# Performance work log

Hardware: AMD Instinct MI355X
Metric: run time of the kernel (lower is better)

Reference implementation:

```python
import jax, jax.numpy as jnp
import numpy as np


def setup_inputs() -> dict:
    key = jax.random.key(0)
    ks = jax.random.split(key, 8)
    B, S, H = 16, 512, 1024
    K, E, L = 32, 1024, 2  # max_node_length, max_edge_length=K**2, num_labels
    seq = jax.random.normal(ks[0], (B, S, H), jnp.float32)
    # structured cumulative proof offsets: col0=1 ('<s>' offset, skipped by forward),
    # then n increasing offsets, zeros terminate. n <= K-1 so NAF node fits in K slots.
    rng = np.random.default_rng(0)
    off = np.zeros((B, K), np.int64)
    off[:, 0] = 1
    for b in range(B):
        n = int(rng.integers(8, K))  # 8..31 segment nodes
        lens = rng.integers(4, 14, size=n)
        off[b, 1:n + 1] = np.cumsum(lens)  # max < 31*13+1 < S
    s = 0.02
    w = lambda k, shp: jax.random.normal(k, shp, jnp.float32) * s
    return {
        'sequence_outputs': seq,
        'proof_offsets': jnp.asarray(off),
        'naf_W': w(ks[1], (H, H)), 'naf_b': jnp.zeros((H,), jnp.float32),
        'cls_dense_W': w(ks[2], (H, H)), 'cls_dense_b': jnp.zeros((H,), jnp.float32),
        'cls_out_W': w(ks[3], (H, L)), 'cls_out_b': jnp.zeros((L,), jnp.float32),
        'node_dense_W': w(ks[4], (H, H)), 'node_dense_b': jnp.zeros((H,), jnp.float32),
        'node_out_W': w(ks[5], (H, L)), 'node_out_b': jnp.zeros((L,), jnp.float32),
        'edge_dense_W': w(ks[6], (3 * H, H)), 'edge_dense_b': jnp.zeros((H,), jnp.float32),
        'edge_out_W': w(ks[7], (H, L)), 'edge_out_b': jnp.zeros((L,), jnp.float32),
        'max_node_length': K,
        'max_edge_length': E,
    }


def _head(x, dW, db, oW, ob):
    # dropout is identity in eval mode
    return jnp.tanh(x @ dW + db) @ oW + ob


def reference(sequence_outputs, proof_offsets,
              naf_W, naf_b, cls_dense_W, cls_dense_b, cls_out_W, cls_out_b,
              node_dense_W, node_dense_b, node_out_W, node_out_b,
              edge_dense_W, edge_dense_b, edge_out_W, edge_out_b,
              max_node_length, max_edge_length):
    B, S, H = sequence_outputs.shape
    K = max_node_length
    E = max_edge_length
    cls_tok = sequence_outputs[:, 0, :]                      # [B,H]
    naf = cls_tok @ naf_W + naf_b                            # [B,H]
    logits = _head(cls_tok, cls_dense_W, cls_dense_b, cls_out_W, cls_out_b)  # [B,L]

    # segment-mean pooling over variable-length spans
    off = proof_offsets[:, 1:]                               # [B,K-1] cumulative offsets
    valid = off > 0                                          # [B,K-1]
    n = valid.sum(axis=1)                                    # [B] #segment nodes
    starts = jnp.concatenate([jnp.ones((B, 1), off.dtype), off[:, :-1] + 1], axis=1)
    pos = jnp.arange(S)
    mask = ((pos[None, None, :] >= starts[:, :, None])
            & (pos[None, None, :] <= off[:, :, None])
            & valid[:, :, None]).astype(sequence_outputs.dtype)  # [B,K-1,S]
    sums = jnp.einsum('bks,bsh->bkh', mask, sequence_outputs)
    counts = mask.sum(axis=-1, keepdims=True)
    node_emb = sums / jnp.maximum(counts, 1.0)               # [B,K-1,H]

    # place segment nodes in slots [0,n), NAF at slot n, zeros after (padded batch buffer)
    slots = jnp.arange(K)
    is_naf = slots[None, :] == n[:, None]
    is_node = slots[None, :] < n[:, None]
    node_emb_p = jnp.pad(node_emb, ((0, 0), (0, 1), (0, 0)))  # [B,K,H]
    full_nodes = jnp.where(is_naf[:, :, None], naf[:, None, :],
                           jnp.where(is_node[:, :, None], node_emb_p, 0.0))  # [B,K,H]

    node_logits = _head(full_nodes, node_dense_W, node_dense_b, node_out_W, node_out_b)

    # pairwise edge features, row-major flattened per sample with m=n+1 nodes:
    # edge[i*m+j] = [node[j], node[i], node[j]-node[i]]
    m = n + 1                                                # [B]
    e = jnp.arange(E)
    i_idx = e[None, :] // m[:, None]                         # [B,E]
    j_idx = e[None, :] % m[:, None]
    valid_e = e[None, :] < (m * m)[:, None]
    i_c = jnp.clip(i_idx, 0, K - 1)
    j_c = jnp.clip(j_idx, 0, K - 1)
    ni = jnp.take_along_axis(full_nodes, i_c[:, :, None], axis=1)  # [B,E,H]
    nj = jnp.take_along_axis(full_nodes, j_c[:, :, None], axis=1)
    edge_feat = jnp.where(valid_e[:, :, None],
                          jnp.concatenate([nj, ni, nj - ni], axis=-1), 0.0)  # [B,E,3H]

    edge_logits = _head(edge_feat, edge_dense_W, edge_dense_b, edge_out_W, edge_out_b)

    return logits, node_logits, edge_logits
```

## Files before the change

kernel.cpp:

```cpp
#include <hip/hip_runtime.h>
#include <hip/hip_bf16.h>

typedef __hip_bfloat16 bf16;
typedef unsigned short ushort;
typedef __attribute__((ext_vector_type(8))) short short8v;
typedef __attribute__((ext_vector_type(4))) float float4v;

__device__ __forceinline__ float us2f(unsigned int u) {
    union { unsigned int i; float f; } c; c.i = u << 16; return c.f;
}
__device__ __forceinline__ bf16 f2bf(float x) { return __float2bfloat16(x); }
__device__ __forceinline__ ushort f2bfu(float x) {
    union { float f; unsigned int i; } c; c.f = x;
    unsigned int lsb = (c.i >> 16) & 1;
    return (ushort)((c.i + 0x7FFF + lsb) >> 16);
}
__device__ __forceinline__ float fcf(float x) {
    return fminf(1000.f, fmaxf(-1000.f, x));
}
__device__ __forceinline__ int iclamp(int v, int lo, int hi) {
    return v < lo ? lo : (v > hi ? hi : v);
}

__device__ __forceinline__ int po_ps(const int* po) {
    return ((po[1] | po[3] | po[5]) == 0) ? 2 : 1;
}
__device__ __forceinline__ int count_n(const int* po, int b, int ps) {
    int n = 0;
    #pragma unroll
    for (int j = 1; j < 32; ++j) n += (po[(b * 32 + j) * ps] > 0) ? 1 : 0;
    return iclamp(n, 0, 31);
}

__global__ __launch_bounds__(256) void k_sentinel(float* __restrict__ out, int nv, float val) {
    int i = blockIdx.x * 256 + threadIdx.x;
    if (i < nv) out[i] = val;
}

__global__ __launch_bounds__(256) void k_prep(const float* __restrict__ ndW,
                                              const float* __restrict__ eW,
                                              ushort* __restrict__ Wct)
{
    const int kt = blockIdx.x, nt = blockIdx.y, z = blockIdx.z;
    const int tid = threadIdx.x;
    __shared__ float T[32][33];

    const int k_loc = tid >> 3, n0 = (tid & 7) * 4;
    const size_t gofs = (size_t)(kt * 32 + k_loc) * 1024 + nt * 32 + n0;
    float4 v;
    if (z == 0) {
        v = *(const float4*)(ndW + gofs);
    } else if (z == 1) {
        float4 a = *(const float4*)(eW + gofs);
        float4 b = *(const float4*)(eW + (size_t)2048 * 1024 + gofs);
        v = make_float4(a.x + b.x, a.y + b.y, a.z + b.z, a.w + b.w);
    } else {
        float4 a = *(const float4*)(eW + (size_t)1024 * 1024 + gofs);
        float4 b = *(const float4*)(eW + (size_t)2048 * 1024 + gofs);
        v = make_float4(a.x - b.x, a.y - b.y, a.z - b.z, a.w - b.w);
    }
    T[k_loc][n0 + 0] = v.x; T[k_loc][n0 + 1] = v.y;
    T[k_loc][n0 + 2] = v.z; T[k_loc][n0 + 3] = v.w;
    __syncthreads();

    const int n_loc = tid >> 3, k0 = (tid & 7) * 4;
    ushort* dst = Wct + (size_t)z * 1024 * 1024 + (size_t)(nt * 32 + n_loc) * 1024 + kt * 32 + k0;
    ushort4 o;
    o.x = f2bfu(T[k0 + 0][n_loc]); o.y = f2bfu(T[k0 + 1][n_loc]);
    o.z = f2bfu(T[k0 + 2][n_loc]); o.w = f2bfu(T[k0 + 3][n_loc]);
    *(ushort4*)dst = o;
}

__global__ __launch_bounds__(256) void k_nodes(const float* __restrict__ seq,
                                               const int* __restrict__ po,
                                               bf16* __restrict__ fn,
                                               int bbase)
{
    const int b_loc = blockIdx.x >> 5;
    const int k = blockIdx.x & 31;
    const int b = bbase + b_loc;
    const int tid = threadIdx.x;
    const int ps = po_ps(po);
    const int n = count_n(po, b, ps);

    const int h0 = tid * 4;
    float4 acc = make_float4(0.f, 0.f, 0.f, 0.f);
    if (k < n) {
        int s_end   = iclamp(po[(b * 32 + k + 1) * ps], 1, 511);
        int s_begin = (k == 0) ? 1 : iclamp(po[(b * 32 + k) * ps] + 1, 1, 511);
        if (s_end < s_begin) s_end = s_begin;
        const float inv = 1.0f / (float)(s_end - s_begin + 1);
        for (int s = s_begin; s <= s_end; ++s) {
            float4 u = *(const float4*)(seq + ((size_t)(b * 512 + s)) * 1024 + h0);
            acc.x += u.x; acc.y += u.y; acc.z += u.z; acc.w += u.w;
        }
        acc.x *= inv; acc.y *= inv; acc.z *= inv; acc.w *= inv;
    }
    bf16* dst = fn + (size_t)(b_loc * 32 + k) * 1024 + h0;
    dst[0] = f2bf(acc.x); dst[1] = f2bf(acc.y); dst[2] = f2bf(acc.z); dst[3] = f2bf(acc.w);
}

__global__ __launch_bounds__(256) void k_cls(const float* __restrict__ seq,
                                             const int* __restrict__ po,
                                             const float* __restrict__ nafW, const float* __restrict__ nafb,
                                             const float* __restrict__ clsW, const float* __restrict__ clsb,
                                             const float* __restrict__ clsoW,
                                             bf16* __restrict__ fn,
                                             float* __restrict__ cacc,
                                             int bbase)
{
    const int b_loc = blockIdx.x, q = blockIdx.y, tid = threadIdx.x;
    const int b = bbase + b_loc;
    const int c = tid & 63, kq = tid >> 6;
    const int hout = q * 64 + c;
    __shared__ float xs[1024];
    __shared__ float red[8][64];
    for (int j = tid; j < 1024; j += 256) xs[j] = seq[(size_t)b * 524288 + j];
    __syncthreads();

    float ca = 0.f, na = 0.f;
    const int kb = kq * 256;
    for (int i = 0; i < 256; ++i) {
        const int k = kb + i;
        float x = xs[k];
        ca = fmaf(x, clsW[(size_t)k * 1024 + hout], ca);
        na = fmaf(x, nafW[(size_t)k * 1024 + hout], na);
    }
    red[kq][c] = ca; red[4 + kq][c] = na;
    __syncthreads();
    if (kq == 0) {
        ca = red[0][c] + red[1][c] + red[2][c] + red[3][c];
        na = red[4][c] + red[5][c] + red[6][c] + red[7][c];
        const int ps = po_ps(po);
        const int n = count_n(po, b, ps);
        fn[(size_t)(b_loc * 32 + n) * 1024 + hout] = f2bf(na + nafb[hout]);
        float h = tanhf(ca + clsb[hout]);
        float2 ow = ((const float2*)clsoW)[hout];
        float q0 = h * ow.x, q1 = h * ow.y;
        #pragma unroll
        for (int off = 32; off > 0; off >>= 1) {
            q0 += __shfl_down(q0, off, 64);
            q1 += __shfl_down(q1, off, 64);
        }
        if (c == 0) {
            atomicAdd(&cacc[b_loc * 2 + 0], q0);
            atomicAdd(&cacc[b_loc * 2 + 1], q1);
        }
    }
}

__global__ __launch_bounds__(256) void k_huv_mfma(const bf16* __restrict__ X,
                                                  const ushort* __restrict__ Wct,
                                                  const float* __restrict__ ndb,
                                                  const float* __restrict__ noW,
                                                  float* __restrict__ nacc,
                                                  bf16* __restrict__ U,
                                                  bf16* __restrict__ V)
{
    const int rt = blockIdx.x;
    const int cc = blockIdx.y;
    const int z  = blockIdx.z;
    const int tid = threadIdx.x;
    const int w = tid >> 6, lane = tid & 63;
    const int quad = lane >> 4, l16 = lane & 15;
    const int rbase = rt * 16;

    __shared__ char smem[32768];
    short* A_lds = (short*)smem;
    float* Rs    = (float*)smem;

    {
        const int r = tid >> 4, s = tid & 15;
        const ushort* src = (const ushort*)X + (size_t)(rbase + r) * 1024 + s * 64;
        #pragma unroll
        for (int cch = 0; cch < 8; ++cch) {
            const int k0 = s * 64 + cch * 8;
            uint4 v = *(const uint4*)(src + cch * 8);
            const int slot = ((k0 >> 5) * 64 + ((k0 >> 3) & 3) * 16 + r) * 8;
            *(uint4*)&A_lds[slot] = v;
        }
    }
    __syncthreads();

    const ushort* Wz = Wct + (size_t)z * 1024 * 1024;
    const int nbase = cc * 128 + w * 32;
    const ushort* B0 = Wz + (size_t)(nbase + l16) * 1024 + quad * 8;
    const ushort* B1 = B0 + (size_t)16 * 1024;

    float4v acc0 = {0.f, 0.f, 0.f, 0.f};
    float4v acc1 = {0.f, 0.f, 0.f, 0.f};

    #pragma unroll 4
    for (int ks = 0; ks < 1024; ks += 32) {
        short8v a  = *(const short8v*)&A_lds[((ks >> 5) * 64 + quad * 16 + l16) * 8];
        short8v b0 = *(const short8v*)(B0 + ks);
        short8v b1 = *(const short8v*)(B1 + ks);
        acc0 = __builtin_amdgcn_mfma_f32_16x16x32_bf16(a, b0, acc0, 0, 0, 0);
        acc1 = __builtin_amdgcn_mfma_f32_16x16x32_bf16(a, b1, acc1, 0, 0, 0);
    }
    __syncthreads();

    #pragma unroll
    for (int reg = 0; reg < 4; ++reg) {
        Rs[(quad * 4 + reg) * 128 + w * 32 + l16]      = acc0[reg];
        Rs[(quad * 4 + reg) * 128 + w * 32 + 16 + l16] = acc1[reg];
    }
    __syncthreads();

    const int row = tid >> 4;
    const int c0 = (tid & 15) * 8;
    const int gcol0 = cc * 128 + c0;
    const float* src = &Rs[row * 128 + c0];
    float s[8];
    {
        float4 a = ((const float4*)src)[0];
        float4 b = ((const float4*)src)[1];
        s[0] = a.x; s[1] = a.y; s[2] = a.z; s[3] = a.w;
        s[4] = b.x; s[5] = b.y; s[6] = b.z; s[7] = b.w;
    }
    if (z == 0) {
        float q0 = 0.f, q1 = 0.f;
        #pragma unroll
        for (int e = 0; e < 8; ++e) {
            float t = tanhf(s[e] + ndb[gcol0 + e]);
            float2 ow = ((const float2*)noW)[gcol0 + e];
            q0 = fmaf(t, ow.x, q0);
            q1 = fmaf(t, ow.y, q1);
        }
        #pragma unroll
        for (int off = 8; off > 0; off >>= 1) {
            q0 += __shfl_down(q0, off, 16);
            q1 += __shfl_down(q1, off, 16);
        }
        if ((tid & 15) == 0) {
            atomicAdd(&nacc[(size_t)(rbase + row) * 2 + 0], q0);
            atomicAdd(&nacc[(size_t)(rbase + row) * 2 + 1], q1);
        }
    } else {
        bf16* dstbuf = (z == 1) ? U : V;
        bf16* dst = dstbuf + (size_t)(rbase + row) * 1024 + gcol0;
        #pragma unroll
        for (int e = 0; e < 8; ++e) dst[e] = f2bf(s[e]);
    }
}

__global__ __launch_bounds__(256) void k_huv_valu(const bf16* __restrict__ X,
                                                  const float* __restrict__ ndW, const float* __restrict__ ndb,
                                                  const float* __restrict__ noW,
                                                  const float* __restrict__ eW,
                                                  float* __restrict__ nacc,
                                                  bf16* __restrict__ U,
                                                  bf16* __restrict__ V)
{
    const int rt = blockIdx.x, cc = blockIdx.y, z = blockIdx.z;
    const int tid = threadIdx.x;
    const int w = tid >> 6, lane = tid & 63;
    const int rg = lane >> 4, cg = lane & 15;
    const int rbase = rt * 16;
    const int colb = cc * 128 + cg * 8;

    __shared__ float LDSb[8192];
    float* Xs = LDSb;
    float* Rs = LDSb;

    const float* W0;
    const float* W1 = nullptr;
    float sgn = 1.f;
    if (z == 0)      { W0 = ndW; }
    else if (z == 1) { W0 = eW; W1 = eW + (size_t)2048 * 1024; }
    else             { W0 = eW + (size_t)1024 * 1024; W1 = eW + (size_t)2048 * 1024; sgn = -1.f; }

    float acc[32];
    #pragma unroll
    for (int i = 0; i < 32; ++i) acc[i] = 0.f;

    const int sr = tid & 15, sq0 = tid >> 4;
    const ushort* Xu = (const ushort*)X;

    for (int ks = 0; ks < 1024; ks += 256) {
        __syncthreads();
        #pragma unroll
        for (int it = 0; it < 4; ++it) {
            int qq = sq0 + it * 16;
            ushort4 xv = *(const ushort4*)(Xu + (size_t)(rbase + sr) * 1024 + ks + qq * 4);
            int kk = qq * 4;
            Xs[(kk + 0) * 16 + sr] = us2f(xv.x);
            Xs[(kk + 1) * 16 + sr] = us2f(xv.y);
            Xs[(kk + 2) * 16 + sr] = us2f(xv.z);
            Xs[(kk + 3) * 16 + sr] = us2f(xv.w);
        }
        __syncthreads();
        const int k0 = ks + w * 64;
        for (int kk = 0; kk < 64; ++kk) {
            float4 xv = *(const float4*)&Xs[(w * 64 + kk) * 16 + rg * 4];
            const float* wp0 = W0 + (size_t)(k0 + kk) * 1024 + colb;
            float4 wa = ((const float4*)wp0)[0];
            float4 wb = ((const float4*)wp0)[1];
            if (W1) {
                const float* wp1 = W1 + (size_t)(k0 + kk) * 1024 + colb;
                float4 va = ((const float4*)wp1)[0];
                float4 vb = ((const float4*)wp1)[1];
                wa.x = fmaf(sgn, va.x, wa.x); wa.y = fmaf(sgn, va.y, wa.y);
                wa.z = fmaf(sgn, va.z, wa.z); wa.w = fmaf(sgn, va.w, wa.w);
                wb.x = fmaf(sgn, vb.x, wb.x); wb.y = fmaf(sgn, vb.y, wb.y);
                wb.z = fmaf(sgn, vb.z, wb.z); wb.w = fmaf(sgn, vb.w, wb.w);
            }
            float xr[4] = {xv.x, xv.y, xv.z, xv.w};
            #pragma unroll
            for (int rr = 0; rr < 4; ++rr) {
                acc[rr*8+0] = fmaf(xr[rr], wa.x, acc[rr*8+0]);
                acc[rr*8+1] = fmaf(xr[rr], wa.y, acc[rr*8+1]);
                acc[rr*8+2] = fmaf(xr[rr], wa.z, acc[rr*8+2]);
                acc[rr*8+3] = fmaf(xr[rr], wa.w, acc[rr*8+3]);
                acc[rr*8+4] = fmaf(xr[rr], wb.x, acc[rr*8+4]);
                acc[rr*8+5] = fmaf(xr[rr], wb.y, acc[rr*8+5]);
                acc[rr*8+6] = fmaf(xr[rr], wb.z, acc[rr*8+6]);
                acc[rr*8+7] = fmaf(xr[rr], wb.w, acc[rr*8+7]);
            }
        }
    }
    __syncthreads();
    #pragma unroll
    for (int rr = 0; rr < 4; ++rr) {
        float* dst = &Rs[w * 2048 + (rg * 4 + rr) * 128 + cg * 8];
        *(float4*)(dst)     = make_float4(acc[rr*8+0], acc[rr*8+1], acc[rr*8+2], acc[rr*8+3]);
        *(float4*)(dst + 4) = make_float4(acc[rr*8+4], acc[rr*8+5], acc[rr*8+6], acc[rr*8+7]);
    }
    __syncthreads();
    const int row = tid >> 4;
    const int c0 = (tid & 15) * 8;
    float s[8];
    #pragma unroll
    for (int e = 0; e < 8; ++e) s[e] = 0.f;
    #pragma unroll
    for (int ww = 0; ww < 4; ++ww) {
        const float* src = &Rs[ww * 2048 + row * 128 + c0];
        float4 a = ((const float4*)src)[0];
        float4 b = ((const float4*)src)[1];
        s[0] += a.x; s[1] += a.y; s[2] += a.z; s[3] += a.w;
        s[4] += b.x; s[5] += b.y; s[6] += b.z; s[7] += b.w;
    }
    const int gcol0 = cc * 128 + c0;
    if (z == 0) {
        float q0 = 0.f, q1 = 0.f;
        #pragma unroll
        for (int e = 0; e < 8; ++e) {
            float t = tanhf(s[e] + ndb[gcol0 + e]);
            float2 ow = ((const float2*)noW)[gcol0 + e];
            q0 = fmaf(t, ow.x, q0);
            q1 = fmaf(t, ow.y, q1);
        }
        #pragma unroll
        for (int off = 8; off > 0; off >>= 1) {
            q0 += __shfl_down(q0, off, 16);
            q1 += __shfl_down(q1, off, 16);
        }
        if ((tid & 15) == 0) {
            atomicAdd(&nacc[(size_t)(rbase + row) * 2 + 0], q0);
            atomicAdd(&nacc[(size_t)(rbase + row) * 2 + 1], q1);
        }
    } else {
        bf16* dstbuf = (z == 1) ? U : V;
        bf16* dst = dstbuf + (size_t)(rbase + row) * 1024 + gcol0;
        #pragma unroll
        for (int e = 0; e < 8; ++e) dst[e] = f2bf(s[e]);
    }
}

__global__ __launch_bounds__(256) void k_fin(const float* __restrict__ nacc,
                                             const float* __restrict__ cacc,
                                             const float* __restrict__ nob,
                                             const float* __restrict__ clsob,
                                             float* __restrict__ out,
                                             int bbase, int nb)
{
    const int idx = blockIdx.x * 256 + threadIdx.x;
    const int nn = nb * 64;
    if (idx < nn) {
        out[32 + bbase * 64 + idx] = fcf(nacc[idx] + nob[idx & 1]);
    } else if (idx < nn + nb * 2) {
        const int c = idx - nn;
        out[(bbase + (c >> 1)) * 2 + (c & 1)] = fcf(cacc[c] + clsob[c & 1]);
    }
}

__global__ __launch_bounds__(256) void k_edge(const bf16* __restrict__ U,
                                              const bf16* __restrict__ V,
                                              const float* __restrict__ edb,
                                              const float* __restrict__ eoW, const float* __restrict__ eob,
                                              const int* __restrict__ po,
                                              float* __restrict__ out,
                                              int bbase)
{
    const int blk = blockIdx.x;
    const int b_loc = blk >> 8;
    const int b = bbase + b_loc;
    const int tid = threadIdx.x;
    const int w = tid >> 6, lane = tid & 63;
    const int e = (blk & 255) * 4 + w;
    const int ps = po_ps(po);
    const int n = count_n(po, b, ps);
    const int m = n + 1;
    const bool valid = e < m * m;
    int i = 0, j = 0;
    if (valid) { i = e / m; j = e - i * m; }
    i = iclamp(i, 0, 31); j = iclamp(j, 0, 31);

    const ushort* urow = (const ushort*)U + (size_t)(b_loc * 32 + j) * 1024;
    const ushort* vrow = (const ushort*)V + (size_t)(b_loc * 32 + i) * 1024;

    float a0 = 0.f, a1 = 0.f;
    #pragma unroll
    for (int c = 0; c < 16; ++c) {
        const int idx = c * 64 + lane;
        float p = edb[idx];
        if (valid) p += us2f(urow[idx]) + us2f(vrow[idx]);
        float t = tanhf(p);
        float2 ow = ((const float2*)eoW)[idx];
        a0 = fmaf(t, ow.x, a0);
        a1 = fmaf(t, ow.y, a1);
    }
    #pragma unroll
    for (int off = 32; off > 0; off >>= 1) {
        a0 += __shfl_down(a0, off, 64);
        a1 += __shfl_down(a1, off, 64);
    }
    if (lane == 0) {
        const size_t o = 32 + 1024 + (size_t)(b * 1024 + e) * 2;
        out[o + 0] = fcf(a0 + eob[0]);
        out[o + 1] = fcf(a1 + eob[1]);
    }
}

extern "C" void kernel_launch(void* const* d_in, const int* in_sizes, int n_in,
                              void* d_out, int out_size, void* d_ws, size_t ws_size,
                              hipStream_t stream) {
    (void)out_size;
    float* out = (float*)d_out;

    bool ok = (n_in >= 16)
        && in_sizes[0] == 8388608 && in_sizes[1] == 512
        && in_sizes[2] == 1048576 && in_sizes[3] == 1024
        && in_sizes[4] == 1048576 && in_sizes[5] == 1024
        && in_sizes[6] == 2048    && in_sizes[7] == 2
        && in_sizes[8] == 1048576 && in_sizes[9] == 1024
        && in_sizes[10] == 2048   && in_sizes[11] == 2
        && in_sizes[12] == 3145728 && in_sizes[13] == 1024
        && in_sizes[14] == 2048   && in_sizes[15] == 2;
    if (!ok) {
        hipLaunchKernelGGL(k_sentinel, dim3(133), dim3(256), 0, stream, out, 33824, 111.0f);
        return;
    }

    const float* seq   = (const float*)d_in[0];
    const int*   po    = (const int*)d_in[1];
    const float* nafW  = (const float*)d_in[2];
    const float* nafb  = (const float*)d_in[3];
    const float* clsW  = (const float*)d_in[4];
    const float* clsb  = (const float*)d_in[5];
    const float* clsoW = (const float*)d_in[6];
    const float* clsob = (const float*)d_in[7];
    const float* ndW   = (const float*)d_in[8];
    const float* ndb   = (const float*)d_in[9];
    const float* noW   = (const float*)d_in[10];
    const float* nob   = (const float*)d_in[11];
    const float* eW    = (const float*)d_in[12];
    const float* edb   = (const float*)d_in[13];
    const float* eoW   = (const float*)d_in[14];
    const float* eob   = (const float*)d_in[15];

    char* ws = (char*)d_ws;

    const size_t fnB  = (size_t)512 * 1024 * 2;
    const size_t accB = 8192;
    const size_t wctB = (size_t)3 * 1024 * 1024 * 2;
    const size_t needA = 3 * fnB + accB + wctB;
    const size_t needB = 3 * fnB + 16 * 66 * sizeof(float);
    const size_t fnC = (size_t)32 * 1024 * 2;
    const size_t needC = 3 * fnC + 66 * sizeof(float);

    if (ws_size >= needA) {
        bf16*   fn   = (bf16*)(ws);
        bf16*   U    = (bf16*)(ws + fnB);
        bf16*   V    = (bf16*)(ws + 2 * fnB);
        float*  nacc = (float*)(ws + 3 * fnB);
        float*  cacc = nacc + 1024;
        ushort* Wct  = (ushort*)(ws + 3 * fnB + accB);
        hipMemsetAsync(nacc, 0, (1024 + 32) * sizeof(float), stream);
        hipLaunchKernelGGL(k_prep, dim3(32, 32, 3), dim3(256), 0, stream, ndW, eW, Wct);
        hipLaunchKernelGGL(k_nodes, dim3(512), dim3(256), 0, stream, seq, po, fn, 0);
        hipLaunchKernelGGL(k_cls, dim3(16, 16), dim3(256), 0, stream,
                           seq, po, nafW, nafb, clsW, clsb, clsoW, fn, cacc, 0);
        hipLaunchKernelGGL(k_huv_mfma, dim3(32, 8, 3), dim3(256), 0, stream,
                           fn, Wct, ndb, noW, nacc, U, V);
        hipLaunchKernelGGL(k_fin, dim3(5), dim3(256), 0, stream, nacc, cacc, nob, clsob, out, 0, 16);
        hipLaunchKernelGGL(k_edge, dim3(4096), dim3(256), 0, stream,
                           U, V, edb, eoW, eob, po, out, 0);
    } else if (ws_size >= needB) {
        bf16*  fn   = (bf16*)(ws);
        bf16*  U    = (bf16*)(ws + fnB);
        bf16*  V    = (bf16*)(ws + 2 * fnB);
        float* nacc = (float*)(ws + 3 * fnB);
        float* cacc = nacc + 1024;
        hipMemsetAsync(nacc, 0, (1024 + 32) * sizeof(float), stream);
        hipLaunchKernelGGL(k_nodes, dim3(512), dim3(256), 0, stream, seq, po, fn, 0);
        hipLaunchKernelGGL(k_cls, dim3(16, 16), dim3(256), 0, stream,
                           seq, po, nafW, nafb, clsW, clsb, clsoW, fn, cacc, 0);
        hipLaunchKernelGGL(k_huv_valu, dim3(32, 8, 3), dim3(256), 0, stream,
                           fn, ndW, ndb, noW, eW, nacc, U, V);
        hipLaunchKernelGGL(k_fin, dim3(5), dim3(256), 0, stream, nacc, cacc, nob, clsob, out, 0, 16);
        hipLaunchKernelGGL(k_edge, dim3(4096), dim3(256), 0, stream,
                           U, V, edb, eoW, eob, po, out, 0);
    } else if (ws_size >= needC) {
        bf16*  fn   = (bf16*)(ws);
        bf16*  U    = (bf16*)(ws + fnC);
        bf16*  V    = (bf16*)(ws + 2 * fnC);
        float* nacc = (float*)(ws + 3 * fnC);
        float* cacc = nacc + 64;
        for (int b = 0; b < 16; ++b) {
            hipMemsetAsync(nacc, 0, 66 * sizeof(float), stream);
            hipLaunchKernelGGL(k_nodes, dim3(32), dim3(256), 0, stream, seq, po, fn, b);
            hipLaunchKernelGGL(k_cls, dim3(1, 16), dim3(256), 0, stream,
                               seq, po, nafW, nafb, clsW, clsb, clsoW, fn, cacc, b);
            hipLaunchKernelGGL(k_huv_valu, dim3(2, 8, 3), dim3(256), 0, stream,
                               fn, ndW, ndb, noW, eW, nacc, U, V);
            hipLaunchKernelGGL(k_fin, dim3(1), dim3(256), 0, stream, nacc, cacc, nob, clsob, out, b, 1);
            hipLaunchKernelGGL(k_edge, dim3(256), dim3(256), 0, stream,
                               U, V, edb, eoW, eob, po, out, b);
        }
    } else {
        hipLaunchKernelGGL(k_sentinel, dim3(133), dim3(256), 0, stream, out, 33824, 222.0f);
    }
}
```

Measured before the change: 207.4 us.

## Fuse prep/nodes/cls into one launch and finalize/edge into another, drop atomics

Merges weight prep, segment pooling and the CLS/NAF projection into one block-partitioned kernel, and merges the node/cls finalization with the edge head into another. The memset and atomics go away: each partial sum gets its own slot and is reduced in the finalize path. Invalid edges reuse a precomputed constant (tanh of the bias dotted with the output weights) instead of running the full loop. This cuts launch count and redundant edge work, but fused blocks of different kinds now share one launch and one shared-memory footprint.

After: 193.2 us. -6.9%, faster.

```diff
diff --git a/kernel.cpp b/kernel.cpp
--- a/kernel.cpp
+++ b/kernel.cpp
@@ -37,13 +37,13 @@
     if (i < nv) out[i] = val;
 }
 
-__global__ __launch_bounds__(256) void k_prep(const float* __restrict__ ndW,
-                                              const float* __restrict__ eW,
-                                              ushort* __restrict__ Wct)
-{
-    const int kt = blockIdx.x, nt = blockIdx.y, z = blockIdx.z;
-    const int tid = threadIdx.x;
-    __shared__ float T[32][33];
+
+__device__ __forceinline__ void dev_prep(int kt, int nt, int z, int tid,
+                                         const float* __restrict__ ndW,
+                                         const float* __restrict__ eW,
+                                         ushort* __restrict__ Wct, float* smemf)
+{
+    float (*T)[33] = (float (*)[33])smemf;
 
     const int k_loc = tid >> 3, n0 = (tid & 7) * 4;
     const size_t gofs = (size_t)(kt * 32 + k_loc) * 1024 + nt * 32 + n0;
@@ -71,17 +71,17 @@
     *(ushort4*)dst = o;
 }
 
-__global__ __launch_bounds__(256) void k_nodes(const float* __restrict__ seq,
-                                               const int* __restrict__ po,
-                                               bf16* __restrict__ fn,
-                                               int bbase)
-{
-    const int b_loc = blockIdx.x >> 5;
-    const int k = blockIdx.x & 31;
+__device__ __forceinline__ void dev_nodes(int bx, int tid,
+                                          const float* __restrict__ seq,
+                                          const int* __restrict__ po,
+                                          bf16* __restrict__ fn, int bbase)
+{
+    const int b_loc = bx >> 5;
+    const int k = bx & 31;
     const int b = bbase + b_loc;
-    const int tid = threadIdx.x;
     const int ps = po_ps(po);
     const int n = count_n(po, b, ps);
+    if (k == n) return;
 
     const int h0 = tid * 4;
     float4 acc = make_float4(0.f, 0.f, 0.f, 0.f);
@@ -100,21 +100,21 @@
     dst[0] = f2bf(acc.x); dst[1] = f2bf(acc.y); dst[2] = f2bf(acc.z); dst[3] = f2bf(acc.w);
 }
 
-__global__ __launch_bounds__(256) void k_cls(const float* __restrict__ seq,
-                                             const int* __restrict__ po,
-                                             const float* __restrict__ nafW, const float* __restrict__ nafb,
-                                             const float* __restrict__ clsW, const float* __restrict__ clsb,
-                                             const float* __restrict__ clsoW,
-                                             bf16* __restrict__ fn,
-                                             float* __restrict__ cacc,
-                                             int bbase)
-{
-    const int b_loc = blockIdx.x, q = blockIdx.y, tid = threadIdx.x;
+__device__ __forceinline__ void dev_cls(int b_loc, int q, int tid,
+                                        const float* __restrict__ seq,
+                                        const int* __restrict__ po,
+                                        const float* __restrict__ nafW, const float* __restrict__ nafb,
+                                        const float* __restrict__ clsW, const float* __restrict__ clsb,
+                                        const float* __restrict__ clsoW,
+                                        bf16* __restrict__ fn,
+                                        float* __restrict__ cacc,
+                                        int bbase, float* smemf)
+{
     const int b = bbase + b_loc;
     const int c = tid & 63, kq = tid >> 6;
     const int hout = q * 64 + c;
-    __shared__ float xs[1024];
-    __shared__ float red[8][64];
+    float* xs  = smemf;
+    float* red = smemf + 1024;
     for (int j = tid; j < 1024; j += 256) xs[j] = seq[(size_t)b * 524288 + j];
     __syncthreads();
 
@@ -126,11 +126,11 @@
         ca = fmaf(x, clsW[(size_t)k * 1024 + hout], ca);
         na = fmaf(x, nafW[(size_t)k * 1024 + hout], na);
     }
-    red[kq][c] = ca; red[4 + kq][c] = na;
+    red[kq * 64 + c] = ca; red[(4 + kq) * 64 + c] = na;
     __syncthreads();
     if (kq == 0) {
-        ca = red[0][c] + red[1][c] + red[2][c] + red[3][c];
-        na = red[4][c] + red[5][c] + red[6][c] + red[7][c];
+        ca = red[0 * 64 + c] + red[1 * 64 + c] + red[2 * 64 + c] + red[3 * 64 + c];
+        na = red[4 * 64 + c] + red[5 * 64 + c] + red[6 * 64 + c] + red[7 * 64 + c];
         const int ps = po_ps(po);
         const int n = count_n(po, b, ps);
         fn[(size_t)(b_loc * 32 + n) * 1024 + hout] = f2bf(na + nafb[hout]);
@@ -143,10 +143,82 @@
             q1 += __shfl_down(q1, off, 64);
         }
         if (c == 0) {
-            atomicAdd(&cacc[b_loc * 2 + 0], q0);
-            atomicAdd(&cacc[b_loc * 2 + 1], q1);
-        }
-    }
+            cacc[(b_loc * 16 + q) * 2 + 0] = q0;
+            cacc[(b_loc * 16 + q) * 2 + 1] = q1;
+        }
+    }
+}
+
+__device__ __forceinline__ void dev_econ(int tid,
+                                         const float* __restrict__ edb,
+                                         const float* __restrict__ eoW,
+                                         float* __restrict__ econ)
+{
+    if (tid >= 64) return;
+    const int lane = tid;
+    float a0 = 0.f, a1 = 0.f;
+    #pragma unroll
+    for (int c = 0; c < 16; ++c) {
+        const int idx = c * 64 + lane;
+        float t = tanhf(edb[idx]);
+        float2 ow = ((const float2*)eoW)[idx];
+        a0 = fmaf(t, ow.x, a0);
+        a1 = fmaf(t, ow.y, a1);
+    }
+    #pragma unroll
+    for (int off = 32; off > 0; off >>= 1) {
+        a0 += __shfl_down(a0, off, 64);
+        a1 += __shfl_down(a1, off, 64);
+    }
+    if (lane == 0) { econ[0] = a0; econ[1] = a1; }
+}
+
+__global__ __launch_bounds__(256) void k_fusedA(const float* __restrict__ seq,
+                                                const int* __restrict__ po,
+                                                const float* __restrict__ nafW, const float* __restrict__ nafb,
+                                                const float* __restrict__ clsW, const float* __restrict__ clsb,
+                                                const float* __restrict__ clsoW,
+                                                const float* __restrict__ ndW,
+                                                const float* __restrict__ eW,
+                                                const float* __restrict__ edb,
+                                                const float* __restrict__ eoW,
+                                                bf16* __restrict__ fn,
+                                                float* __restrict__ cacc,
+                                                ushort* __restrict__ Wct,
+                                                float* __restrict__ econ)
+{
+    __shared__ float smem[1536];
+    const int blk = blockIdx.x;
+    const int tid = threadIdx.x;
+    if (blk < 3072) {
+        const int z = blk >> 10, rem = blk & 1023;
+        dev_prep(rem & 31, rem >> 5, z, tid, ndW, eW, Wct, smem);
+    } else if (blk < 3584) {
+        dev_nodes(blk - 3072, tid, seq, po, fn, 0);
+    } else if (blk < 3840) {
+        const int r = blk - 3584;
+        dev_cls(r & 15, r >> 4, tid, seq, po, nafW, nafb, clsW, clsb, clsoW, fn, cacc, 0, smem);
+    } else {
+        dev_econ(tid, edb, eoW, econ);
+    }
+}
+
+__global__ __launch_bounds__(256) void k_nodes(const float* __restrict__ seq,
+                                               const int* __restrict__ po,
+                                               bf16* __restrict__ fn, int bbase)
+{
+    dev_nodes(blockIdx.x, threadIdx.x, seq, po, fn, bbase);
+}
+__global__ __launch_bounds__(256) void k_cls(const float* __restrict__ seq,
+                                             const int* __restrict__ po,
+                                             const float* __restrict__ nafW, const float* __restrict__ nafb,
+                                             const float* __restrict__ clsW, const float* __restrict__ clsb,
+                                             const float* __restrict__ clsoW,
+                                             bf16* __restrict__ fn,
+                                             float* __restrict__ cacc, int bbase)
+{
+    __shared__ float smem[1536];
+    dev_cls(blockIdx.x, blockIdx.y, threadIdx.x, seq, po, nafW, nafb, clsW, clsb, clsoW, fn, cacc, bbase, smem);
 }
 
 __global__ __launch_bounds__(256) void k_huv_mfma(const bf16* __restrict__ X,
@@ -233,8 +305,8 @@
             q1 += __shfl_down(q1, off, 16);
         }
         if ((tid & 15) == 0) {
-            atomicAdd(&nacc[(size_t)(rbase + row) * 2 + 0], q0);
-            atomicAdd(&nacc[(size_t)(rbase + row) * 2 + 1], q1);
+            float* np = nacc + ((size_t)(rbase + row) * 8 + cc) * 2;
+            np[0] = q0; np[1] = q1;
         }
     } else {
         bf16* dstbuf = (z == 1) ? U : V;
@@ -356,8 +428,8 @@
             q1 += __shfl_down(q1, off, 16);
         }
         if ((tid & 15) == 0) {
-            atomicAdd(&nacc[(size_t)(rbase + row) * 2 + 0], q0);
-            atomicAdd(&nacc[(size_t)(rbase + row) * 2 + 1], q1);
+            float* np = nacc + ((size_t)(rbase + row) * 8 + cc) * 2;
+            np[0] = q0; np[1] = q1;
         }
     } else {
         bf16* dstbuf = (z == 1) ? U : V;
@@ -367,20 +439,28 @@
     }
 }
 
-__global__ __launch_bounds__(256) void k_fin(const float* __restrict__ nacc,
-                                             const float* __restrict__ cacc,
-                                             const float* __restrict__ nob,
-                                             const float* __restrict__ clsob,
-                                             float* __restrict__ out,
-                                             int bbase, int nb)
+__global__ __launch_bounds__(256) void k_fin2(const float* __restrict__ nacc,
+                                              const float* __restrict__ cacc,
+                                              const float* __restrict__ nob,
+                                              const float* __restrict__ clsob,
+                                              float* __restrict__ out,
+                                              int bbase, int nb)
 {
     const int idx = blockIdx.x * 256 + threadIdx.x;
-    const int nn = nb * 64;
-    if (idx < nn) {
-        out[32 + bbase * 64 + idx] = fcf(nacc[idx] + nob[idx & 1]);
-    } else if (idx < nn + nb * 2) {
-        const int c = idx - nn;
-        out[(bbase + (c >> 1)) * 2 + (c & 1)] = fcf(cacc[c] + clsob[c & 1]);
+    const int R = nb * 32;
+    if (idx < R) {
+        const float4* p = (const float4*)(nacc + (size_t)idx * 16);
+        float4 a = p[0], b4 = p[1], c4 = p[2], d4 = p[3];
+        float s0 = a.x + a.z + b4.x + b4.z + c4.x + c4.z + d4.x + d4.z;
+        float s1 = a.y + a.w + b4.y + b4.w + c4.y + c4.w + d4.y + d4.w;
+        out[32 + bbase * 64 + idx * 2 + 0] = fcf(s0 + nob[0]);
+        out[32 + bbase * 64 + idx * 2 + 1] = fcf(s1 + nob[1]);
+    } else if (idx < R + nb * 2) {
+        const int c = idx - R;
+        const int b = c >> 1, l = c & 1;
+        float s = 0.f;
+        for (int q = 0; q < 16; ++q) s += cacc[(b * 16 + q) * 2 + l];
+        out[(bbase + b) * 2 + l] = fcf(s + clsob[l]);
     }
 }
 
@@ -427,6 +507,83 @@
     }
     if (lane == 0) {
         const size_t o = 32 + 1024 + (size_t)(b * 1024 + e) * 2;
+        out[o + 0] = fcf(a0 + eob[0]);
+        out[o + 1] = fcf(a1 + eob[1]);
+    }
+}
+
+__global__ __launch_bounds__(256) void k_fusedC(const bf16* __restrict__ U,
+                                                const bf16* __restrict__ V,
+                                                const float* __restrict__ nacc,
+                                                const float* __restrict__ cacc,
+                                                const float* __restrict__ nob,
+                                                const float* __restrict__ clsob,
+                                                const float* __restrict__ edb,
+                                                const float* __restrict__ eoW,
+                                                const float* __restrict__ eob,
+                                                const float* __restrict__ econ,
+                                                const int* __restrict__ po,
+                                                float* __restrict__ out)
+{
+    const int blk = blockIdx.x;
+    const int tid = threadIdx.x;
+
+    if (blk >= 4096) {
+        const int idx = (blk - 4096) * 256 + tid;
+        if (idx < 512) {
+            const float4* p = (const float4*)(nacc + (size_t)idx * 16);
+            float4 a = p[0], b4 = p[1], c4 = p[2], d4 = p[3];
+            float s0 = a.x + a.z + b4.x + b4.z + c4.x + c4.z + d4.x + d4.z;
+            float s1 = a.y + a.w + b4.y + b4.w + c4.y + c4.w + d4.y + d4.w;
+            out[32 + idx * 2 + 0] = fcf(s0 + nob[0]);
+            out[32 + idx * 2 + 1] = fcf(s1 + nob[1]);
+        } else if (idx < 544) {
+            const int c = idx - 512;
+            const int b = c >> 1, l = c & 1;
+            float s = 0.f;
+            for (int q = 0; q < 16; ++q) s += cacc[(b * 16 + q) * 2 + l];
+            out[b * 2 + l] = fcf(s + clsob[l]);
+        }
+        return;
+    }
+
+    const int b = blk >> 8;
+    const int w = tid >> 6, lane = tid & 63;
+    const int e = (blk & 255) * 4 + w;
+    const int ps = po_ps(po);
+    const int n = count_n(po, b, ps);
+    const int m = n + 1;
+    const size_t o = 32 + 1024 + (size_t)(b * 1024 + e) * 2;
+
+    if (e >= m * m) {
+        if (lane == 0) {
+            out[o + 0] = fcf(econ[0] + eob[0]);
+            out[o + 1] = fcf(econ[1] + eob[1]);
+        }
+        return;
+    }
+
+    int i = e / m, j = e - i * m;
+    i = iclamp(i, 0, 31); j = iclamp(j, 0, 31);
+    const ushort* urow = (const ushort*)U + (size_t)(b * 32 + j) * 1024;
+    const ushort* vrow = (const ushort*)V + (size_t)(b * 32 + i) * 1024;
+
+    float a0 = 0.f, a1 = 0.f;
+    #pragma unroll
+    for (int c = 0; c < 16; ++c) {
+        const int idx = c * 64 + lane;
+        float p = edb[idx] + us2f(urow[idx]) + us2f(vrow[idx]);
+        float t = tanhf(p);
+        float2 ow = ((const float2*)eoW)[idx];
+        a0 = fmaf(t, ow.x, a0);
+        a1 = fmaf(t, ow.y, a1);
+    }
+    #pragma unroll
+    for (int off = 32; off > 0; off >>= 1) {
+        a0 += __shfl_down(a0, off, 64);
+        a1 += __shfl_down(a1, off, 64);
+    }
+    if (lane == 0) {
         out[o + 0] = fcf(a0 + eob[0]);
         out[o + 1] = fcf(a1 + eob[1]);
     }
@@ -471,44 +628,43 @@
 
     char* ws = (char*)d_ws;
 
-    const size_t fnB  = (size_t)512 * 1024 * 2;
-    const size_t accB = 8192;
-    const size_t wctB = (size_t)3 * 1024 * 1024 * 2;
-    const size_t needA = 3 * fnB + accB + wctB;
-    const size_t needB = 3 * fnB + 16 * 66 * sizeof(float);
-    const size_t fnC = (size_t)32 * 1024 * 2;
-    const size_t needC = 3 * fnC + 66 * sizeof(float);
+    const size_t fnB   = (size_t)512 * 1024 * 2;
+    const size_t naccB = (size_t)512 * 8 * 2 * sizeof(float);
+    const size_t caccB = (size_t)16 * 16 * 2 * sizeof(float);
+    const size_t econB = 64;
+    const size_t wctB  = (size_t)3 * 1024 * 1024 * 2;
+    const size_t needA = 3 * fnB + naccB + caccB + econB + wctB;
+    const size_t needB = 3 * fnB + naccB + caccB;
+    const size_t fnC   = (size_t)32 * 1024 * 2;
+    const size_t needC = 3 * fnC + (size_t)32 * 8 * 2 * sizeof(float) + (size_t)16 * 2 * sizeof(float);
 
     if (ws_size >= needA) {
         bf16*   fn   = (bf16*)(ws);
         bf16*   U    = (bf16*)(ws + fnB);
         bf16*   V    = (bf16*)(ws + 2 * fnB);
         float*  nacc = (float*)(ws + 3 * fnB);
-        float*  cacc = nacc + 1024;
-        ushort* Wct  = (ushort*)(ws + 3 * fnB + accB);
-        hipMemsetAsync(nacc, 0, (1024 + 32) * sizeof(float), stream);
-        hipLaunchKernelGGL(k_prep, dim3(32, 32, 3), dim3(256), 0, stream, ndW, eW, Wct);
-        hipLaunchKernelGGL(k_nodes, dim3(512), dim3(256), 0, stream, seq, po, fn, 0);
-        hipLaunchKernelGGL(k_cls, dim3(16, 16), dim3(256), 0, stream,
-                           seq, po, nafW, nafb, clsW, clsb, clsoW, fn, cacc, 0);
+        float*  cacc = (float*)(ws + 3 * fnB + naccB);
+        float*  econ = (float*)(ws + 3 * fnB + naccB + caccB);
+        ushort* Wct  = (ushort*)(ws + 3 * fnB + naccB + caccB + econB);
+        hipLaunchKernelGGL(k_fusedA, dim3(3841), dim3(256), 0, stream,
+                           seq, po, nafW, nafb, clsW, clsb, clsoW, ndW, eW, edb, eoW,
+                           fn, cacc, Wct, econ);
         hipLaunchKernelGGL(k_huv_mfma, dim3(32, 8, 3), dim3(256), 0, stream,
                            fn, Wct, ndb, noW, nacc, U, V);
-        hipLaunchKernelGGL(k_fin, dim3(5), dim3(256), 0, stream, nacc, cacc, nob, clsob, out, 0, 16);
-        hipLaunchKernelGGL(k_edge, dim3(4096), dim3(256), 0, stream,
-                           U, V, edb, eoW, eob, po, out, 0);
+        hipLaunchKernelGGL(k_fusedC, dim3(4099), dim3(256), 0, stream,
+                           U, V, nacc, cacc, nob, clsob, edb, eoW, eob, econ, po, out);
     } else if (ws_size >= needB) {
         bf16*  fn   = (bf16*)(ws);
         bf16*  U    = (bf16*)(ws + fnB);
         bf16*  V    = (bf16*)(ws + 2 * fnB);
         float* nacc = (float*)(ws + 3 * fnB);
-        float* cacc = nacc + 1024;
-        hipMemsetAsync(nacc, 0, (1024 + 32) * sizeof(float), stream);
+        float* cacc = (float*)(ws + 3 * fnB + naccB);
         hipLaunchKernelGGL(k_nodes, dim3(512), dim3(256), 0, stream, seq, po, fn, 0);
         hipLaunchKernelGGL(k_cls, dim3(16, 16), dim3(256), 0, stream,
                            seq, po, nafW, nafb, clsW, clsb, clsoW, fn, cacc, 0);
         hipLaunchKernelGGL(k_huv_valu, dim3(32, 8, 3), dim3(256), 0, stream,
                            fn, ndW, ndb, noW, eW, nacc, U, V);
-        hipLaunchKernelGGL(k_fin, dim3(5), dim3(256), 0, stream, nacc, cacc, nob, clsob, out, 0, 16);
+        hipLaunchKernelGGL(k_fin2, dim3(3), dim3(256), 0, stream, nacc, cacc, nob, clsob, out, 0, 16);
         hipLaunchKernelGGL(k_edge, dim3(4096), dim3(256), 0, stream,
                            U, V, edb, eoW, eob, po, out, 0);
     } else if (ws_size >= needC) {
@@ -516,15 +672,14 @@
         bf16*  U    = (bf16*)(ws + fnC);
         bf16*  V    = (bf16*)(ws + 2 * fnC);
         float* nacc = (float*)(ws + 3 * fnC);
-        float* cacc = nacc + 64;
+        float* cacc = nacc + 32 * 8 * 2;
         for (int b = 0; b < 16; ++b) {
-            hipMemsetAsync(nacc, 0, 66 * sizeof(float), stream);
             hipLaunchKernelGGL(k_nodes, dim3(32), dim3(256), 0, stream, seq, po, fn, b);
             hipLaunchKernelGGL(k_cls, dim3(1, 16), dim3(256), 0, stream,
                                seq, po, nafW, nafb, clsW, clsb, clsoW, fn, cacc, b);
             hipLaunchKernelGGL(k_huv_valu, dim3(2, 8, 3), dim3(256), 0, stream,
                                fn, ndW, ndb, noW, eW, nacc, U, V);
-            hipLaunchKernelGGL(k_fin, dim3(1), dim3(256), 0, stream, nacc, cacc, nob, clsob, out, b, 1);
+            hipLaunchKernelGGL(k_fin2, dim3(1), dim3(256), 0, stream, nacc, cacc, nob, clsob, out, b, 1);
             hipLaunchKernelGGL(k_edge, dim3(256), dim3(256), 0, stream,
                                U, V, edb, eoW, eob, po, out, b);
         }
```
